# Optimization experiments

Hardware: AMD Instinct MI355X
Metric: run time of the kernel (lower is better)

Reference implementation:

```python
import jax, jax.numpy as jnp
import numpy as np

B, L, S, D, H, CTX = 2, 2048, 512, 1024, 16, 1024
HD = D // H
HID = 4 * D
EPS = 1e-6


def _ln(x):
    mu = jnp.mean(x, axis=-1, keepdims=True)
    var = jnp.mean((x - mu) ** 2, axis=-1, keepdims=True)
    return (x - mu) * jax.lax.rsqrt(var + EPS)


def _rotate_half(x):
    x1, x2 = jnp.split(x, 2, axis=-1)
    return jnp.concatenate([-x2, x1], axis=-1)


def _heads(t):  # [B,N,D] -> [B,H,N,HD]
    return t.reshape(t.shape[0], t.shape[1], H, HD).transpose(0, 2, 1, 3)


def _merge(t):  # [B,H,N,HD] -> [B,N,D]
    return t.transpose(0, 2, 1, 3).reshape(t.shape[0], t.shape[2], D)


def setup_inputs() -> dict:
    key = jax.random.key(0)
    ks = jax.random.split(key, 24)
    s = 0.02
    inp = {
        "x": jax.random.normal(ks[0], (B, L, D), jnp.float32),
        "timestep_emb": jax.random.normal(ks[1], (B, D), jnp.float32),
        "context_emb": jax.random.normal(ks[2], (B, S, CTX), jnp.float32),
        "rope_emb": jax.random.normal(ks[3], (L, HD), jnp.float32),
        # adaLN modulation: Linear(D -> 6D) with bias
        "w_mod": jax.random.normal(ks[4], (D, 6 * D), jnp.float32) * s,
        "b_mod": jnp.zeros((6 * D,), jnp.float32),
        # self-attention (no qkv bias, out has bias)
        "wq_s": jax.random.normal(ks[5], (D, D), jnp.float32) * s,
        "wk_s": jax.random.normal(ks[6], (D, D), jnp.float32) * s,
        "wv_s": jax.random.normal(ks[7], (D, D), jnp.float32) * s,
        "wo_s": jax.random.normal(ks[8], (D, D), jnp.float32) * s,
        "bo_s": jnp.zeros((D,), jnp.float32),
        # cross-attention (q/k/v no bias, out has bias)
        "wq_c": jax.random.normal(ks[9], (D, D), jnp.float32) * s,
        "wk_c": jax.random.normal(ks[10], (CTX, D), jnp.float32) * s,
        "wv_c": jax.random.normal(ks[11], (CTX, D), jnp.float32) * s,
        "wo_c": jax.random.normal(ks[12], (D, D), jnp.float32) * s,
        "bo_c": jnp.zeros((D,), jnp.float32),
        # MLP
        "w1": jax.random.normal(ks[13], (D, HID), jnp.float32) * s,
        "b1": jnp.zeros((HID,), jnp.float32),
        "w2": jax.random.normal(ks[14], (HID, D), jnp.float32) * s,
        "b2": jnp.zeros((D,), jnp.float32),
    }
    return inp


def reference(x, timestep_emb, context_emb, rope_emb,
              w_mod, b_mod,
              wq_s, wk_s, wv_s, wo_s, bo_s,
              wq_c, wk_c, wv_c, wo_c, bo_c,
              w1, b1, w2, b2):
    scale = HD ** -0.5
    # adaLN modulation from timestep embedding
    mods = jnp.split(timestep_emb @ w_mod + b_mod, 6, axis=-1)
    shift_msa, scale_msa, gate_msa, shift_mlp, scale_mlp, gate_mlp = mods

    # --- self-attention with RoPE ---
    nx = _ln(x) * (1.0 + scale_msa[:, None, :]) + shift_msa[:, None, :]
    q = _heads(nx @ wq_s)
    k = _heads(nx @ wk_s)
    v = _heads(nx @ wv_s)
    cos = jnp.cos(rope_emb)[None, None]  # [1,1,L,HD]
    sin = jnp.sin(rope_emb)[None, None]
    q = q * cos + _rotate_half(q) * sin
    k = k * cos + _rotate_half(k) * sin
    attn = jax.nn.softmax(jnp.einsum("bhqd,bhkd->bhqk", q, k) * scale, axis=-1)
    sa = _merge(jnp.einsum("bhqk,bhkd->bhqd", attn, v)) @ wo_s + bo_s
    x = x + gate_msa[:, None, :] * sa

    # --- cross-attention (no mask) ---
    nx = _ln(x)
    q = _heads(nx @ wq_c)
    k = _heads(context_emb @ wk_c)
    v = _heads(context_emb @ wv_c)
    attn = jax.nn.softmax(jnp.einsum("bhqd,bhkd->bhqk", q, k) * scale, axis=-1)
    ca = _merge(jnp.einsum("bhqk,bhkd->bhqd", attn, v)) @ wo_c + bo_c
    x = x + ca

    # --- MLP with modulation + gate ---
    nx = _ln(x) * (1.0 + scale_mlp[:, None, :]) + shift_mlp[:, None, :]
    h = jax.nn.gelu(nx @ w1 + b1, approximate=False)
    x = x + gate_mlp[:, None, :] * (h @ w2 + b2)
    return x
```

## Files before the change

kernel.cpp:

```cpp
#include <hip/hip_runtime.h>
#include <hip/hip_bf16.h>


typedef short short8 __attribute__((ext_vector_type(8)));
typedef float f32x4 __attribute__((ext_vector_type(4)));
typedef float f32x16 __attribute__((ext_vector_type(16)));

#define DEV __device__ __forceinline__

DEV unsigned short f2b(float f) {
  __hip_bfloat16 h = __float2bfloat16(f);
  return *reinterpret_cast<unsigned short*>(&h);
}
DEV float b2f(unsigned short u) {
  unsigned int x = ((unsigned int)u) << 16;
  return __builtin_bit_cast(float, x);
}
DEV unsigned int pk2(float lo, float hi) {
  unsigned int r;
  asm("v_cvt_pk_bf16_f32 %0, %1, %2" : "=v"(r) : "v"(lo), "v"(hi));
  return r;
}
DEV void vpsw(unsigned int& a, unsigned int& b) {
  asm("v_permlane32_swap_b32 %0, %1" : "+v"(a), "+v"(b));
}
DEV float max3f(float a, float b, float c) {
  float r;
  asm("v_max3_f32 %0, %1, %2, %3" : "=v"(r) : "v"(a), "v"(b), "v"(c));
  return r;
}

#define GLB(p) ((const __attribute__((address_space(1))) void*)(p))
#define LDSP(p) ((__attribute__((address_space(3))) void*)(p))

struct TCB { const float* in; unsigned short* out; float scale; };
struct PrepArgs {
  const float* wmod; const float* te; const float* bmod; float* mods;
  TCB sq[8];
  const float* w1; unsigned short* w1T;
  const float* w2; unsigned short* w2T;
  const float* ctx; unsigned short* ctxb;
  const float* rope; float2* cs;
};

__global__ __launch_bounds__(256) void prep(PrepArgs a) {
  __shared__ float t32[32][33];
  __shared__ float tes[2048];
  const int blk = blockIdx.x;
  const int tid = threadIdx.x;
  const int tx = tid & 31, ty = tid >> 5;
  if (blk < 24) {
    const int j = blk * 256 + tid;
    for (int u = tid; u < 2048; u += 256) tes[u] = a.te[u];
    __syncthreads();
    float a0 = 0.f, b0 = 0.f, a1 = 0.f, b1 = 0.f;
#pragma unroll 8
    for (int k = 0; k < 1024; k += 2) {
      float v0 = a.wmod[(size_t)k * 6144 + j];
      float v1 = a.wmod[(size_t)(k + 1) * 6144 + j];
      a0 += tes[k] * v0;
      b0 += tes[k + 1] * v1;
      a1 += tes[1024 + k] * v0;
      b1 += tes[1024 + k + 1] * v1;
    }
    float bm = a.bmod[j];
    a.mods[j] = a0 + b0 + bm;
    a.mods[6144 + j] = a1 + b1 + bm;
  } else if (blk < 16408) {
    const float* in;
    unsigned short* out;
    int R, C, gx, tile;
    float scale;
    if (blk < 8216) {
      int j = (blk - 24) >> 10;
      tile = (blk - 24) & 1023;
      in = a.sq[j].in; out = a.sq[j].out; scale = a.sq[j].scale;
      R = 1024; C = 1024; gx = 32;
    } else if (blk < 12312) {
      tile = blk - 8216;
      in = a.w1; out = a.w1T; R = 1024; C = 4096; gx = 128; scale = 1.f;
    } else {
      tile = blk - 12312;
      in = a.w2; out = a.w2T; R = 4096; C = 1024; gx = 32; scale = 1.f;
    }
    int bx = (tile % gx) * 32, by = (tile / gx) * 32;
#pragma unroll
    for (int i = ty; i < 32; i += 8)
      t32[i][tx] = in[(size_t)(by + i) * C + bx + tx];
    __syncthreads();
#pragma unroll
    for (int i = ty; i < 32; i += 8)
      out[(size_t)(bx + i) * R + by + tx] = f2b(t32[tx][i] * scale);
  } else if (blk < 18456) {
    int i = (blk - 16408) * 512 + tid * 2;
    float2 v = *(const float2*)&a.ctx[i];
    *(unsigned int*)&a.ctxb[i] = pk2(v.x, v.y);
  } else {
    int i = (blk - 18456) * 256 + tid;
    float v = a.rope[i];
    a.cs[i] = make_float2(cosf(v), sinf(v));
  }
}

template <int BF16IN>
__global__ __launch_bounds__(256) void ln_mod(
    const void* __restrict__ xin, const float* __restrict__ mods,
    unsigned short* __restrict__ out, int scale_ofs, int shift_ofs) {
  int row = blockIdx.x;
  int b = row >> 11;
  int tid = threadIdx.x;
  float vv[4];
  if constexpr (BF16IN) {
    const unsigned short* xr = (const unsigned short*)xin + (size_t)row * 1024;
    ushort4 u = ((const ushort4*)xr)[tid];
    vv[0] = b2f(u.x); vv[1] = b2f(u.y); vv[2] = b2f(u.z); vv[3] = b2f(u.w);
  } else {
    const float* xr = (const float*)xin + (size_t)row * 1024;
    float4 v = ((const float4*)xr)[tid];
    vv[0] = v.x; vv[1] = v.y; vv[2] = v.z; vv[3] = v.w;
  }
  float s = vv[0] + vv[1] + vv[2] + vv[3];
  float ss = vv[0] * vv[0] + vv[1] * vv[1] + vv[2] * vv[2] + vv[3] * vv[3];
#pragma unroll
  for (int off = 32; off >= 1; off >>= 1) {
    s += __shfl_down(s, off);
    ss += __shfl_down(ss, off);
  }
  __shared__ float red[8];
  int wave = tid >> 6, lane = tid & 63;
  if (lane == 0) { red[wave] = s; red[4 + wave] = ss; }
  __syncthreads();
  if (tid == 0) {
    float S = red[0] + red[1] + red[2] + red[3];
    float SS = red[4] + red[5] + red[6] + red[7];
    float mu = S * (1.f / 1024.f);
    red[0] = mu;
    red[1] = SS * (1.f / 1024.f) - mu * mu;
  }
  __syncthreads();
  float mu = red[0];
  float rs = rsqrtf(red[1] + 1e-6f);
  unsigned short o[4];
#pragma unroll
  for (int c = 0; c < 4; ++c) {
    int col = tid * 4 + c;
    float nv = (vv[c] - mu) * rs;
    if (scale_ofs >= 0)
      nv = nv * (1.f + mods[(size_t)b * 6144 + scale_ofs + col]) +
           mods[(size_t)b * 6144 + shift_ofs + col];
    o[c] = f2b(nv);
  }
  *(ushort4*)(&out[(size_t)row * 1024 + tid * 4]) = *(const ushort4*)o;
}

template <int EPI, int MI, int NJ>
DEV void gemm_epilogue(f32x4 (&acc)[MI][NJ], void* Cout, const float* bias,
                       const float* mods, int gate_ofs, const float* src,
                       int N, int rowsPerB, int m0, int n0, int wm, int wn,
                       int g, int r) {
#pragma unroll
  for (int i = 0; i < MI; ++i) {
#pragma unroll
    for (int j = 0; j < NJ; ++j) {
#pragma unroll
      for (int q = 0; q < 4; ++q) {
        size_t grow = (size_t)(m0 + wm + i * 16 + g * 4 + q);
        size_t gcol = (size_t)(n0 + wn + j * 16 + r);
        float v = acc[i][j][q];
        if constexpr (EPI == 0) {
          ((unsigned short*)Cout)[grow * N + gcol] = f2b(v);
        } else if constexpr (EPI == 1) {
          v += bias[gcol];
          float ge = 0.5f * v * (1.0f + erff(v * 0.70710678f));
          ((unsigned short*)Cout)[grow * N + gcol] = f2b(ge);
        } else if constexpr (EPI == 3) {
          size_t buf = gcol >> 10;
          ((unsigned short*)Cout)[buf * (4096ull * 1024) + grow * 1024 + (gcol & 1023)] = f2b(v);
        } else if constexpr (EPI == 5) {
          v += bias[gcol];
          float gate = 1.0f;
          if (gate_ofs >= 0)
            gate = mods[(grow / rowsPerB) * 6144 + gate_ofs + gcol];
          ((unsigned short*)Cout)[grow * N + gcol] =
              f2b(src[grow * N + gcol] + gate * v);
        } else if constexpr (EPI == 7) {
          v += bias[gcol];
          float gate = 1.0f;
          if (gate_ofs >= 0)
            gate = mods[(grow / rowsPerB) * 6144 + gate_ofs + gcol];
          float sv = b2f(((const unsigned short*)src)[grow * N + gcol]);
          ((float*)Cout)[grow * N + gcol] = sv + gate * v;
        } else {
          v += bias[gcol];
          float gate = 1.0f;
          if (gate_ofs >= 0)
            gate = mods[(grow / rowsPerB) * 6144 + gate_ofs + gcol];
          ((float*)Cout)[grow * N + gcol] = src[grow * N + gcol] + gate * v;
        }
      }
    }
  }
}

DEV void qkv_rope_epilogue(f32x4 (&acc)[4][4], unsigned short* Cout,
                           const float2* cs, int m0, int n0, int wm, int wn,
                           int g, int r) {
  const int buf = (n0 + wn) >> 10;
  const int colbase = (n0 + wn) & 1023;
  unsigned short* base = Cout + (size_t)buf * (4096ull * 1024);
#pragma unroll
  for (int i = 0; i < 4; ++i) {
#pragma unroll
    for (int q = 0; q < 4; ++q) {
      size_t grow = (size_t)(m0 + wm + i * 16 + g * 4 + q);
      unsigned short* orow = base + grow * 1024 + colbase + r;
      if (buf < 2) {
        int l = (int)(grow & 2047);
#pragma unroll
        for (int j = 0; j < 2; ++j) {
          int d = j * 16 + r;
          float2 a = cs[l * 64 + d];
          float2 bb = cs[l * 64 + d + 32];
          float x1 = acc[i][j][q], x2 = acc[i][j + 2][q];
          orow[j * 16] = f2b(x1 * a.x - x2 * a.y);
          orow[(j + 2) * 16] = f2b(x2 * bb.x + x1 * bb.y);
        }
      } else {
#pragma unroll
        for (int j = 0; j < 4; ++j) orow[j * 16] = f2b(acc[i][j][q]);
      }
    }
  }
}

template <int EPI>
__global__ __launch_bounds__(256, 2) void gemm_bt(
    const unsigned short* __restrict__ A, const unsigned short* __restrict__ Bt,
    void* __restrict__ Cout, const float* __restrict__ bias,
    const float* __restrict__ mods, int gate_ofs, const float* __restrict__ src,
    int M, int N, int K, int rowsPerB) {
  __shared__ unsigned short As[128 * 32];
  __shared__ unsigned short Bs[128 * 32];
  const int tid = threadIdx.x;
  const int wave = tid >> 6, lane = tid & 63;
  const int g = lane >> 4, r = lane & 15;
  const int m0 = blockIdx.y * 128, n0 = blockIdx.x * 128;
  const int wm = (wave >> 1) * 64, wn = (wave & 1) * 64;
  const int srow = lane >> 2;
  const int scol = (lane & 3) * 8;

  f32x4 acc[4][4] = {};

  for (int k0 = 0; k0 < K; k0 += 32) {
    __syncthreads();
#pragma unroll
    for (int cc = 0; cc < 4; ++cc) {
      int c = wave * 4 + cc;
      int isB = c >> 3;
      int cl = c & 7;
      int row = cl * 16 + srow;
      const unsigned short* gsrc =
          isB ? (Bt + (size_t)(n0 + row) * K + k0 + scol)
              : (A + (size_t)(m0 + row) * K + k0 + scol);
      unsigned short* ldst = (isB ? Bs : As) + cl * 512;
      __builtin_amdgcn_global_load_lds(GLB(gsrc), LDSP(ldst), 16, 0, 0);
    }
    __syncthreads();

    short8 bfr[4];
#pragma unroll
    for (int j = 0; j < 4; ++j)
      bfr[j] = *(const short8*)(&Bs[(wn + j * 16 + r) * 32 + g * 8]);
#pragma unroll
    for (int i = 0; i < 4; ++i) {
      short8 af = *(const short8*)(&As[(wm + i * 16 + r) * 32 + g * 8]);
#pragma unroll
      for (int j = 0; j < 4; ++j)
        acc[i][j] = __builtin_amdgcn_mfma_f32_16x16x32_bf16(af, bfr[j], acc[i][j], 0, 0, 0);
    }
  }
  gemm_epilogue<EPI, 4, 4>(acc, Cout, bias, mods, gate_ofs, src, N, rowsPerB,
                           m0, n0, wm, wn, g, r);
}

template <int EPI>
__global__ __launch_bounds__(256) void gemm_pipe(
    const unsigned short* __restrict__ A, const unsigned short* __restrict__ Bt,
    void* __restrict__ Cout, const float* __restrict__ bias,
    const float* __restrict__ mods, int gate_ofs, const float* __restrict__ src,
    int M, int N, int K, int rowsPerB, int mshift) {
  __shared__ unsigned short lds[4 * 16384];
  const int tid = threadIdx.x;
  const int wave = tid >> 6, lane = tid & 63;
  const int g = lane >> 4, r = lane & 15;
  const int flat = blockIdx.x;
  const int xcd = flat & 7, idx = flat >> 3;
  const int mt = xcd * (1 << mshift) + (idx & ((1 << mshift) - 1));
  const int nt = idx >> mshift;
  const int m0 = mt * 128, n0 = nt * 128;
  const int wm = (wave >> 1) * 64, wn = (wave & 1) * 64;
  const int srow8 = lane >> 3;
  const int sck = (lane & 7) ^ srow8;

  f32x4 acc[4][4] = {};

  auto stage = [&](int t, int bufi) {
    const int k0 = t * 64;
#pragma unroll
    for (int i = 0; i < 8; ++i) {
      int u = wave * 8 + i;
      int isB = u >> 4;
      int uu = u & 15;
      int rl = uu * 8 + srow8;
      const unsigned short* gsrc =
          (isB ? (Bt + (size_t)(n0 + rl) * K) : (A + (size_t)(m0 + rl) * K)) +
          k0 + sck * 8;
      unsigned short* dst = (unsigned short*)lds + bufi * 16384 + isB * 8192 + uu * 512;
      __builtin_amdgcn_global_load_lds(GLB(gsrc), LDSP(dst), 16, 0, 0);
    }
  };

  const int nt_k = K / 64;
  stage(0, 0);
  stage(1, 1);
  stage(2, 2);

  for (int t = 0; t < nt_k; ++t) {
    int rem = nt_k - t;
    if (rem >= 3) {
      asm volatile("s_waitcnt vmcnt(16)" ::: "memory");
    } else if (rem == 2) {
      asm volatile("s_waitcnt vmcnt(8)" ::: "memory");
    } else {
      asm volatile("s_waitcnt vmcnt(0)" ::: "memory");
    }
    __builtin_amdgcn_sched_barrier(0);
    __builtin_amdgcn_s_barrier();
    __builtin_amdgcn_sched_barrier(0);
    if (t + 3 < nt_k) stage(t + 3, (t + 3) & 3);

    const unsigned short* Ab = (const unsigned short*)lds + (t & 3) * 16384;
    const unsigned short* Bb = Ab + 8192;
#pragma unroll
    for (int ks = 0; ks < 2; ++ks) {
      short8 bfr[4];
#pragma unroll
      for (int j = 0; j < 4; ++j) {
        int row = wn + j * 16 + r;
        bfr[j] = *(const short8*)&Bb[row * 64 + ((g + ks * 4) ^ (r & 7)) * 8];
      }
#pragma unroll
      for (int i = 0; i < 4; ++i) {
        int row = wm + i * 16 + r;
        short8 af = *(const short8*)&Ab[row * 64 + ((g + ks * 4) ^ (r & 7)) * 8];
#pragma unroll
        for (int j = 0; j < 4; ++j)
          acc[i][j] = __builtin_amdgcn_mfma_f32_16x16x32_bf16(af, bfr[j], acc[i][j], 0, 0, 0);
      }
    }
  }
  if constexpr (EPI == 4) {
    qkv_rope_epilogue(acc, (unsigned short*)Cout, (const float2*)bias,
                      m0, n0, wm, wn, g, r);
  } else {
    gemm_epilogue<EPI, 4, 4>(acc, Cout, bias, mods, gate_ofs, src, N, rowsPerB,
                             m0, n0, wm, wn, g, r);
  }
}

template <int EPI>
__global__ __launch_bounds__(256) void gemm_p2(
    const unsigned short* __restrict__ A, const unsigned short* __restrict__ Bt,
    void* __restrict__ Cout, const float* __restrict__ bias,
    const float* __restrict__ mods, int gate_ofs, const float* __restrict__ src,
    int M, int N, int K, int rowsPerB, int ntn) {
  __shared__ unsigned short lds[3 * 12288];
  const int tid = threadIdx.x;
  const int wave = tid >> 6, lane = tid & 63;
  const int g = lane >> 4, r = lane & 15;
  const int flat = blockIdx.x;
  const int nt = flat % ntn, mt = flat / ntn;
  const int m0 = mt * 64, n0 = nt * 128;
  const int wm = (wave >> 1) * 32, wn = (wave & 1) * 64;
  const int srow8 = lane >> 3;
  const int sck = (lane & 7) ^ srow8;

  f32x4 acc[2][4] = {};

  auto stage = [&](int t, int bufi) {
    const int k0 = t * 64;
    unsigned short* base = (unsigned short*)lds + bufi * 12288;
#pragma unroll
    for (int i = 0; i < 2; ++i) {
      int u = wave * 2 + i;
      int rl = u * 8 + srow8;
      const unsigned short* gsrc = A + (size_t)(m0 + rl) * K + k0 + sck * 8;
      __builtin_amdgcn_global_load_lds(GLB(gsrc), LDSP(base + u * 512), 16, 0, 0);
    }
#pragma unroll
    for (int i = 0; i < 4; ++i) {
      int u = wave * 4 + i;
      int rl = u * 8 + srow8;
      const unsigned short* gsrc = Bt + (size_t)(n0 + rl) * K + k0 + sck * 8;
      __builtin_amdgcn_global_load_lds(GLB(gsrc), LDSP(base + 4096 + u * 512), 16, 0, 0);
    }
  };

  const int ntk = K / 64;
  stage(0, 0);
  stage(1, 1);
  int cbuf = 0, sbuf = 2;

  for (int t = 0; t < ntk; ++t) {
    if (t < ntk - 1) {
      asm volatile("s_waitcnt vmcnt(6)" ::: "memory");
    } else {
      asm volatile("s_waitcnt vmcnt(0)" ::: "memory");
    }
    __builtin_amdgcn_sched_barrier(0);
    __builtin_amdgcn_s_barrier();
    __builtin_amdgcn_sched_barrier(0);
    if (t + 2 < ntk) {
      stage(t + 2, sbuf);
      sbuf = (sbuf == 2) ? 0 : sbuf + 1;
    }

    const unsigned short* Ab = (const unsigned short*)lds + cbuf * 12288;
    const unsigned short* Bb = Ab + 4096;
#pragma unroll
    for (int ks = 0; ks < 2; ++ks) {
      short8 bfr[4];
#pragma unroll
      for (int j = 0; j < 4; ++j) {
        int row = wn + j * 16 + r;
        bfr[j] = *(const short8*)&Bb[row * 64 + ((g + ks * 4) ^ (r & 7)) * 8];
      }
#pragma unroll
      for (int i = 0; i < 2; ++i) {
        int row = wm + i * 16 + r;
        short8 af = *(const short8*)&Ab[row * 64 + ((g + ks * 4) ^ (r & 7)) * 8];
#pragma unroll
        for (int j = 0; j < 4; ++j)
          acc[i][j] = __builtin_amdgcn_mfma_f32_16x16x32_bf16(af, bfr[j], acc[i][j], 0, 0, 0);
      }
    }
    cbuf = (cbuf == 2) ? 0 : cbuf + 1;
  }
  gemm_epilogue<EPI, 2, 4>(acc, Cout, bias, mods, gate_ofs, src, N, rowsPerB,
                           m0, n0, wm, wn, g, r);
}

__global__ __launch_bounds__(256) void gemm_cross(
    const unsigned short* __restrict__ Anx, const unsigned short* __restrict__ Bq,
    unsigned short* __restrict__ Oq,
    const unsigned short* __restrict__ Actx, const unsigned short* __restrict__ Bkv,
    unsigned short* __restrict__ Okv) {
  __shared__ unsigned short lds[3 * 12288];
  const int tid = threadIdx.x;
  const int wave = tid >> 6, lane = tid & 63;
  const int g = lane >> 4, r = lane & 15;
  const bool iskv = blockIdx.x >= 512;
  const int flat = iskv ? (blockIdx.x - 512) : blockIdx.x;
  const int ntn = iskv ? 16 : 8;
  const unsigned short* A = iskv ? Actx : Anx;
  const unsigned short* Bt = iskv ? Bkv : Bq;
  const int nt = flat % ntn, mt = flat / ntn;
  const int m0 = mt * 64, n0 = nt * 128;
  const int K = 1024;
  const int wm = (wave >> 1) * 32, wn = (wave & 1) * 64;
  const int srow8 = lane >> 3;
  const int sck = (lane & 7) ^ srow8;

  f32x4 acc[2][4] = {};

  auto stage = [&](int t, int bufi) {
    const int k0 = t * 64;
    unsigned short* base = (unsigned short*)lds + bufi * 12288;
#pragma unroll
    for (int i = 0; i < 2; ++i) {
      int u = wave * 2 + i;
      int rl = u * 8 + srow8;
      const unsigned short* gsrc = A + (size_t)(m0 + rl) * K + k0 + sck * 8;
      __builtin_amdgcn_global_load_lds(GLB(gsrc), LDSP(base + u * 512), 16, 0, 0);
    }
#pragma unroll
    for (int i = 0; i < 4; ++i) {
      int u = wave * 4 + i;
      int rl = u * 8 + srow8;
      const unsigned short* gsrc = Bt + (size_t)(n0 + rl) * K + k0 + sck * 8;
      __builtin_amdgcn_global_load_lds(GLB(gsrc), LDSP(base + 4096 + u * 512), 16, 0, 0);
    }
  };

  const int ntk = K / 64;
  stage(0, 0);
  stage(1, 1);
  int cbuf = 0, sbuf = 2;

  for (int t = 0; t < ntk; ++t) {
    if (t < ntk - 1) {
      asm volatile("s_waitcnt vmcnt(6)" ::: "memory");
    } else {
      asm volatile("s_waitcnt vmcnt(0)" ::: "memory");
    }
    __builtin_amdgcn_sched_barrier(0);
    __builtin_amdgcn_s_barrier();
    __builtin_amdgcn_sched_barrier(0);
    if (t + 2 < ntk) {
      stage(t + 2, sbuf);
      sbuf = (sbuf == 2) ? 0 : sbuf + 1;
    }

    const unsigned short* Ab = (const unsigned short*)lds + cbuf * 12288;
    const unsigned short* Bb = Ab + 4096;
#pragma unroll
    for (int ks = 0; ks < 2; ++ks) {
      short8 bfr[4];
#pragma unroll
      for (int j = 0; j < 4; ++j) {
        int row = wn + j * 16 + r;
        bfr[j] = *(const short8*)&Bb[row * 64 + ((g + ks * 4) ^ (r & 7)) * 8];
      }
#pragma unroll
      for (int i = 0; i < 2; ++i) {
        int row = wm + i * 16 + r;
        short8 af = *(const short8*)&Ab[row * 64 + ((g + ks * 4) ^ (r & 7)) * 8];
#pragma unroll
        for (int j = 0; j < 4; ++j)
          acc[i][j] = __builtin_amdgcn_mfma_f32_16x16x32_bf16(af, bfr[j], acc[i][j], 0, 0, 0);
      }
    }
    cbuf = (cbuf == 2) ? 0 : cbuf + 1;
  }

#pragma unroll
  for (int i = 0; i < 2; ++i) {
#pragma unroll
    for (int j = 0; j < 4; ++j) {
#pragma unroll
      for (int q = 0; q < 4; ++q) {
        size_t grow = (size_t)(m0 + wm + i * 16 + g * 4 + q);
        size_t gcol = (size_t)(n0 + wn + j * 16 + r);
        float v = acc[i][j][q];
        if (iskv) {
          size_t buf = gcol >> 10;
          Okv[buf * (4096ull * 1024) + grow * 1024 + (gcol & 1023)] = f2b(v);
        } else {
          Oq[grow * 1024 + gcol] = f2b(v);
        }
      }
    }
  }
}

__global__ __launch_bounds__(256, 2) void flash2(
    const unsigned short* __restrict__ Q, const unsigned short* __restrict__ Kv,
    const unsigned short* __restrict__ Vv, unsigned short* __restrict__ O,
    int Lk) {
  __shared__ unsigned short lds[20480];
  const int tid = threadIdx.x, wave = tid >> 6, lane = tid & 63;
  const int hi = lane >> 5, lq = lane & 31;
  const int flat = blockIdx.x;
  const int xcd = flat & 7, rr = flat >> 3;
  const int gl = rr >> 4, qt = rr & 15;
  const int g = xcd * 4 + gl;
  const int h = g & 15, b = g >> 4;
  const int Lq = 2048, D = 1024;

  const unsigned short* Qbase =
      Q + ((size_t)b * Lq + qt * 128 + wave * 32 + lq) * D + h * 64;
  const unsigned short* Kbase = Kv + (size_t)b * Lk * D + h * 64;
  const unsigned short* Vbase = Vv + (size_t)b * Lk * D + h * 64;

  short8 qf[4];
#pragma unroll
  for (int kb = 0; kb < 4; ++kb)
    qf[kb] = *(const short8*)(Qbase + kb * 16 + hi * 8);

  const short8 ones = {0x3F80, 0x3F80, 0x3F80, 0x3F80, 0x3F80, 0x3F80, 0x3F80, 0x3F80};
  const f32x16 z16 = {};

  const int kr0 = tid >> 3, kc0 = tid & 7;
  const int kvp = tid >> 3, db = tid & 7;
  const int kch0 = (kc0 ^ (kr0 & 7) ^ (kr0 >> 3)) & 7;
  const int kch1 = kch0 ^ 4;
  const int f0 = (lq & 7) ^ (lq >> 3);
  const int swz0 = f0 << 4, swz1 = swz0 ^ 64;

  int vby[8];
#pragma unroll
  for (int e = 0; e < 8; ++e) {
    int d = db * 8 + e;
    vby[e] = d * 128 + ((kvp * 4) ^ (((e ^ db) & 7) << 4));
  }

  float m_run = -3.0e38f;
  f32x16 o0 = {}, o1 = {}, lacc = {};
  short8 vr0, vr1;
  short8 pbf[4];

  auto stageK = [&](int t, int bi) {
    const unsigned short* s0 = Kbase + (size_t)(t * 64 + kr0) * D + kch0 * 8;
    const unsigned short* s1 = Kbase + (size_t)(t * 64 + kr0 + 32) * D + kch1 * 8;
    __builtin_amdgcn_global_load_lds(GLB(s0), LDSP(&lds[bi * 4096 + wave * 512]), 16, 0, 0);
    __builtin_amdgcn_global_load_lds(GLB(s1), LDSP(&lds[bi * 4096 + 2048 + wave * 512]), 16, 0, 0);
  };
  auto loadV = [&](int t) {
    const unsigned short* v0 = Vbase + (size_t)(t * 64 + 2 * kvp) * D + db * 8;
    vr0 = *(const short8*)v0;
    vr1 = *(const short8*)(v0 + D);
  };
  auto writeV = [&](int t) {
    char* vt = (char*)&lds[12288 + (t & 1) * 4096];
    union { short8 s; unsigned int u[4]; } a, c;
    a.s = vr0; c.s = vr1;
#pragma unroll
    for (int k = 0; k < 4; ++k) {
      *(unsigned int*)(vt + vby[2 * k]) =
          __builtin_amdgcn_perm(c.u[k], a.u[k], 0x05040100u);
      *(unsigned int*)(vt + vby[2 * k + 1]) =
          __builtin_amdgcn_perm(c.u[k], a.u[k], 0x07060302u);
    }
  };
  auto qk = [&](int bi, f32x16& sa0, f32x16& sa1) {
    const unsigned short* K0 = &lds[bi * 4096];
    {
      int lo = hi * 16;
      short8 a0 = *(const short8*)&K0[lq * 64 + ((lo ^ swz0) >> 1)];
      short8 a1 = *(const short8*)&K0[(32 + lq) * 64 + ((lo ^ swz1) >> 1)];
      sa0 = __builtin_amdgcn_mfma_f32_32x32x16_bf16(a0, qf[0], z16, 0, 0, 0);
      sa1 = __builtin_amdgcn_mfma_f32_32x32x16_bf16(a1, qf[0], z16, 0, 0, 0);
    }
#pragma unroll
    for (int ks = 1; ks < 4; ++ks) {
      int lo = ks * 32 + hi * 16;
      short8 a0 = *(const short8*)&K0[lq * 64 + ((lo ^ swz0) >> 1)];
      short8 a1 = *(const short8*)&K0[(32 + lq) * 64 + ((lo ^ swz1) >> 1)];
      sa0 = __builtin_amdgcn_mfma_f32_32x32x16_bf16(a0, qf[ks], sa0, 0, 0, 0);
      sa1 = __builtin_amdgcn_mfma_f32_32x32x16_bf16(a1, qf[ks], sa1, 0, 0, 0);
    }
  };
  auto finish = [&](f32x16& s0a, f32x16& s1a) {
    float tm[8];
#pragma unroll
    for (int i = 0; i < 8; ++i)
      tm[i] = fmaxf(max3f(s0a[i], s0a[i + 8], s1a[i]), s1a[i + 8]);
    float x = max3f(tm[0], tm[1], tm[2]);
    float y = max3f(tm[3], tm[4], tm[5]);
    float pm = fmaxf(max3f(tm[6], tm[7], x), y);
    {
      unsigned int ua = __builtin_bit_cast(unsigned int, pm), ub = ua;
      vpsw(ua, ub);
      pm = fmaxf(__builtin_bit_cast(float, ua), __builtin_bit_cast(float, ub));
    }
    if (__any(pm - m_run > 8.0f)) {
      float mnew = fmaxf(m_run, pm);
      float alpha = exp2f(m_run - mnew);
      lacc[0] *= alpha;
#pragma unroll
      for (int i = 0; i < 16; ++i) { o0[i] *= alpha; o1[i] *= alpha; }
      m_run = mnew;
    }
    float mc = m_run;
#pragma unroll
    for (int i = 0; i < 16; ++i) s0a[i] = exp2f(s0a[i] - mc);
#pragma unroll
    for (int i = 0; i < 16; ++i) s1a[i] = exp2f(s1a[i] - mc);
#pragma unroll
    for (int kb = 0; kb < 4; ++kb) {
      int bb = (kb & 1) * 8;
      float p0, p1, p2, p3, p4, p5, p6, p7;
      if (kb < 2) {
        p0 = s0a[bb + 0]; p1 = s0a[bb + 1]; p2 = s0a[bb + 2]; p3 = s0a[bb + 3];
        p4 = s0a[bb + 4]; p5 = s0a[bb + 5]; p6 = s0a[bb + 6]; p7 = s0a[bb + 7];
      } else {
        p0 = s1a[bb + 0]; p1 = s1a[bb + 1]; p2 = s1a[bb + 2]; p3 = s1a[bb + 3];
        p4 = s1a[bb + 4]; p5 = s1a[bb + 5]; p6 = s1a[bb + 6]; p7 = s1a[bb + 7];
      }
      unsigned int u0 = pk2(p0, p1), u1 = pk2(p2, p3);
      unsigned int u2 = pk2(p4, p5), u3 = pk2(p6, p7);
      vpsw(u0, u2);
      vpsw(u1, u3);
      union { unsigned int u[4]; short8 s; } fr;
      fr.u[0] = u0; fr.u[1] = u1; fr.u[2] = u2; fr.u[3] = u3;
      pbf[kb] = fr.s;
    }
  };
  auto pv = [&](int t) {
    const unsigned short* V0 = &lds[12288 + (t & 1) * 4096];
    __builtin_amdgcn_s_setprio(1);
#pragma unroll
    for (int kb = 0; kb < 4; ++kb) {
      int lo = kb * 32 + hi * 16;
      short8 vf0 = *(const short8*)&V0[lq * 64 + ((lo ^ swz0) >> 1)];
      short8 vf1 = *(const short8*)&V0[(32 + lq) * 64 + ((lo ^ swz1) >> 1)];
      o0 = __builtin_amdgcn_mfma_f32_32x32x16_bf16(vf0, pbf[kb], o0, 0, 0, 0);
      o1 = __builtin_amdgcn_mfma_f32_32x32x16_bf16(vf1, pbf[kb], o1, 0, 0, 0);
      lacc = __builtin_amdgcn_mfma_f32_32x32x16_bf16(ones, pbf[kb], lacc, 0, 0, 0);
    }
    __builtin_amdgcn_s_setprio(0);
  };

  const int nkt = Lk / 64;

  stageK(0, 0);
  loadV(0);
  writeV(0);
  stageK(1, 1);
  __syncthreads();

  f32x16 sA0, sA1, sB0, sB1;
  qk(0, sA0, sA1);

  auto pstep = [&](int t, f32x16& n0, f32x16& n1, f32x16& p0, f32x16& p1) {
    const int tq = t + 1;
    if (tq < nkt) {
      loadV(tq);
      if (tq + 1 < nkt) stageK(tq + 1, (tq + 1) % 3);
      qk(tq % 3, n0, n1);
    }
    finish(p0, p1);
    if (tq < nkt) writeV(tq);
    pv(t);
    __syncthreads();
  };

  for (int t = 0; t < nkt; t += 2) {
    pstep(t, sB0, sB1, sA0, sA1);
    pstep(t + 1, sA0, sA1, sB0, sB1);
  }

  float rl = 1.0f / lacc[0];
  unsigned short* os = &lds[wave * 2048];
#pragma unroll
  for (int t = 0; t < 2; ++t) {
#pragma unroll
    for (int c = 0; c < 4; ++c) {
      int dbase = 32 * t + 8 * c + 4 * hi;
      float v0 = (t ? o1[4 * c + 0] : o0[4 * c + 0]) * rl;
      float v1 = (t ? o1[4 * c + 1] : o0[4 * c + 1]) * rl;
      float v2 = (t ? o1[4 * c + 2] : o0[4 * c + 2]) * rl;
      float v3 = (t ? o1[4 * c + 3] : o0[4 * c + 3]) * rl;
      int by0 = lq * 128 + ((dbase * 2) ^ ((lq & 7) << 4));
      int by1 = lq * 128 + (((dbase + 2) * 2) ^ ((lq & 7) << 4));
      *(unsigned int*)((char*)os + by0) = pk2(v0, v1);
      *(unsigned int*)((char*)os + by1) = pk2(v2, v3);
    }
  }
  int q2 = lane >> 1;
  unsigned short* orow =
      O + ((size_t)b * Lq + qt * 128 + wave * 32 + q2) * D + h * 64;
#pragma unroll
  for (int j = 0; j < 4; ++j) {
    int j2 = (lane & 1) * 4 + j;
    int byr = q2 * 128 + ((j2 * 16) ^ ((q2 & 7) << 4));
    short8 vv = *(const short8*)((char*)os + byr);
    *(short8*)(orow + j2 * 8) = vv;
  }
}

extern "C" void kernel_launch(void* const* d_in, const int* in_sizes, int n_in,
                              void* d_out, int out_size, void* d_ws, size_t ws_size,
                              hipStream_t stream) {
  (void)in_sizes; (void)n_in; (void)out_size; (void)ws_size;
  const float* x_in = (const float*)d_in[0];
  const float* te   = (const float*)d_in[1];
  const float* ctx  = (const float*)d_in[2];
  const float* rope = (const float*)d_in[3];
  const float* wmod = (const float*)d_in[4];
  const float* bmod = (const float*)d_in[5];
  const float* wqs  = (const float*)d_in[6];
  const float* wks  = (const float*)d_in[7];
  const float* wvs  = (const float*)d_in[8];
  const float* wos  = (const float*)d_in[9];
  const float* bos  = (const float*)d_in[10];
  const float* wqc  = (const float*)d_in[11];
  const float* wkc  = (const float*)d_in[12];
  const float* wvc  = (const float*)d_in[13];
  const float* woc  = (const float*)d_in[14];
  const float* boc  = (const float*)d_in[15];
  const float* w1   = (const float*)d_in[16];
  const float* b1   = (const float*)d_in[17];
  const float* w2   = (const float*)d_in[18];
  const float* b2   = (const float*)d_in[19];
  float* out = (float*)d_out;

  char* w = (char*)d_ws;
  size_t o = 0;
  auto alloc = [&](size_t bytes) {
    char* p = w + o;
    o = (o + bytes + 255) & ~(size_t)255;
    return p;
  };
  unsigned short* wqsT  = (unsigned short*)alloc(1024ull * 1024 * 2);
  unsigned short* wksT  = (unsigned short*)alloc(1024ull * 1024 * 2);
  unsigned short* wvsT  = (unsigned short*)alloc(1024ull * 1024 * 2);
  unsigned short* wosT  = (unsigned short*)alloc(1024ull * 1024 * 2);
  unsigned short* wqcT  = (unsigned short*)alloc(1024ull * 1024 * 2);
  unsigned short* wkcT  = (unsigned short*)alloc(1024ull * 1024 * 2);
  unsigned short* wvcT  = (unsigned short*)alloc(1024ull * 1024 * 2);
  unsigned short* wocT  = (unsigned short*)alloc(1024ull * 1024 * 2);
  unsigned short* w1T   = (unsigned short*)alloc(4096ull * 1024 * 2);
  unsigned short* w2T   = (unsigned short*)alloc(1024ull * 4096 * 2);
  float* modsb = (float*)alloc(2ull * 6144 * 4);
  float2* csT  = (float2*)alloc(2048ull * 64 * 8);
  unsigned short* nx   = (unsigned short*)alloc(4096ull * 1024 * 2);
  unsigned short* ctxb = (unsigned short*)alloc(1024ull * 1024 * 2);
  unsigned short* qb = (unsigned short*)alloc(4096ull * 1024 * 2);
  unsigned short* kb = (unsigned short*)alloc(4096ull * 1024 * 2);
  unsigned short* vb = (unsigned short*)alloc(4096ull * 1024 * 2);
  unsigned short* ao = (unsigned short*)alloc(4096ull * 1024 * 2);
  unsigned short* xwb = (unsigned short*)alloc(4096ull * 1024 * 2);
  float* xw = (float*)alloc(4096ull * 1024 * 4);
  unsigned short* hbuf = qb;

  const float c1 = 0.125f * 1.4426950408889634f;

  PrepArgs pa;
  pa.wmod = wmod; pa.te = te; pa.bmod = bmod; pa.mods = modsb;
  pa.sq[0] = {wqs, wqsT, c1};
  pa.sq[1] = {wks, wksT, 1.0f};
  pa.sq[2] = {wvs, wvsT, 1.0f};
  pa.sq[3] = {wos, wosT, 1.0f};
  pa.sq[4] = {wqc, wqcT, 1.0f};
  pa.sq[5] = {wkc, wkcT, c1};
  pa.sq[6] = {wvc, wvcT, 1.0f};
  pa.sq[7] = {woc, wocT, 1.0f};
  pa.w1 = w1; pa.w1T = w1T;
  pa.w2 = w2; pa.w2T = w2T;
  pa.ctx = ctx; pa.ctxb = ctxb;
  pa.rope = rope; pa.cs = csT;
  prep<<<18968, 256, 0, stream>>>(pa);

  ln_mod<0><<<4096, 256, 0, stream>>>(x_in, modsb, nx, 1024, 0);
  gemm_pipe<4><<<768, 256, 0, stream>>>(nx, wqsT, qb, (const float*)csT, nullptr, -1, nullptr, 4096, 3072, 1024, 2048, 2);
  flash2<<<512, 256, 0, stream>>>(qb, kb, vb, ao, 2048);
  gemm_p2<5><<<512, 256, 0, stream>>>(ao, wosT, xwb, bos, modsb, 2048, x_in, 4096, 1024, 1024, 2048, 8);

  ln_mod<1><<<4096, 256, 0, stream>>>(xwb, modsb, nx, -1, -1);
  gemm_cross<<<768, 256, 0, stream>>>(nx, wqcT, qb, ctxb, wkcT, kb);
  flash2<<<512, 256, 0, stream>>>(qb, kb, vb, ao, 512);
  gemm_p2<7><<<512, 256, 0, stream>>>(ao, wocT, xw, boc, modsb, -1, (const float*)xwb, 4096, 1024, 1024, 2048, 8);

  ln_mod<0><<<4096, 256, 0, stream>>>(xw, modsb, nx, 4096, 3072);
  gemm_bt<1><<<dim3(32, 32), 256, 0, stream>>>(nx, w1T, hbuf, b1, nullptr, -1, nullptr, 4096, 4096, 1024, 2048);
  gemm_p2<2><<<512, 256, 0, stream>>>(hbuf, w2T, out, b2, modsb, 5120, xw, 4096, 1024, 4096, 2048, 8);
}
```

Measured before the change: 387.2 us.

## Compute cross-attention K/V projection inside self-attention flash kernel as extra blocks

The context K/V projection depends only on the context embedding, so it now runs as 128 extra blocks appended to the self-attention flash kernel launch. Those blocks do a simple 128x128-tiled GEMM and write into new dedicated kc/vc buffers. The Q-only cross projection then uses the existing gemm_p2 kernel, and the separate gemm_cross launch is dropped. This overlaps the small K/V GEMM with attention and shortens the work between LN and cross-attention, at the cost of a less pipelined, single-buffered GEMM path and LDS/register pressure inside flash2.

```diff
diff --git a/kernel.cpp b/kernel.cpp
--- a/kernel.cpp
+++ b/kernel.cpp
@@ -450,115 +450,70 @@
                            m0, n0, wm, wn, g, r);
 }
 
-__global__ __launch_bounds__(256) void gemm_cross(
-    const unsigned short* __restrict__ Anx, const unsigned short* __restrict__ Bq,
-    unsigned short* __restrict__ Oq,
-    const unsigned short* __restrict__ Actx, const unsigned short* __restrict__ Bkv,
-    unsigned short* __restrict__ Okv) {
-  __shared__ unsigned short lds[3 * 12288];
-  const int tid = threadIdx.x;
-  const int wave = tid >> 6, lane = tid & 63;
-  const int g = lane >> 4, r = lane & 15;
-  const bool iskv = blockIdx.x >= 512;
-  const int flat = iskv ? (blockIdx.x - 512) : blockIdx.x;
-  const int ntn = iskv ? 16 : 8;
-  const unsigned short* A = iskv ? Actx : Anx;
-  const unsigned short* Bt = iskv ? Bkv : Bq;
-  const int nt = flat % ntn, mt = flat / ntn;
-  const int m0 = mt * 64, n0 = nt * 128;
-  const int K = 1024;
-  const int wm = (wave >> 1) * 32, wn = (wave & 1) * 64;
-  const int srow8 = lane >> 3;
-  const int sck = (lane & 7) ^ srow8;
-
-  f32x4 acc[2][4] = {};
-
-  auto stage = [&](int t, int bufi) {
-    const int k0 = t * 64;
-    unsigned short* base = (unsigned short*)lds + bufi * 12288;
-#pragma unroll
-    for (int i = 0; i < 2; ++i) {
-      int u = wave * 2 + i;
-      int rl = u * 8 + srow8;
-      const unsigned short* gsrc = A + (size_t)(m0 + rl) * K + k0 + sck * 8;
-      __builtin_amdgcn_global_load_lds(GLB(gsrc), LDSP(base + u * 512), 16, 0, 0);
-    }
-#pragma unroll
-    for (int i = 0; i < 4; ++i) {
-      int u = wave * 4 + i;
-      int rl = u * 8 + srow8;
-      const unsigned short* gsrc = Bt + (size_t)(n0 + rl) * K + k0 + sck * 8;
-      __builtin_amdgcn_global_load_lds(GLB(gsrc), LDSP(base + 4096 + u * 512), 16, 0, 0);
-    }
-  };
-
-  const int ntk = K / 64;
-  stage(0, 0);
-  stage(1, 1);
-  int cbuf = 0, sbuf = 2;
-
-  for (int t = 0; t < ntk; ++t) {
-    if (t < ntk - 1) {
-      asm volatile("s_waitcnt vmcnt(6)" ::: "memory");
-    } else {
-      asm volatile("s_waitcnt vmcnt(0)" ::: "memory");
-    }
-    __builtin_amdgcn_sched_barrier(0);
-    __builtin_amdgcn_s_barrier();
-    __builtin_amdgcn_sched_barrier(0);
-    if (t + 2 < ntk) {
-      stage(t + 2, sbuf);
-      sbuf = (sbuf == 2) ? 0 : sbuf + 1;
-    }
-
-    const unsigned short* Ab = (const unsigned short*)lds + cbuf * 12288;
-    const unsigned short* Bb = Ab + 4096;
-#pragma unroll
-    for (int ks = 0; ks < 2; ++ks) {
-      short8 bfr[4];
-#pragma unroll
-      for (int j = 0; j < 4; ++j) {
-        int row = wn + j * 16 + r;
-        bfr[j] = *(const short8*)&Bb[row * 64 + ((g + ks * 4) ^ (r & 7)) * 8];
-      }
-#pragma unroll
-      for (int i = 0; i < 2; ++i) {
-        int row = wm + i * 16 + r;
-        short8 af = *(const short8*)&Ab[row * 64 + ((g + ks * 4) ^ (r & 7)) * 8];
-#pragma unroll
-        for (int j = 0; j < 4; ++j)
-          acc[i][j] = __builtin_amdgcn_mfma_f32_16x16x32_bf16(af, bfr[j], acc[i][j], 0, 0, 0);
-      }
-    }
-    cbuf = (cbuf == 2) ? 0 : cbuf + 1;
-  }
-
-#pragma unroll
-  for (int i = 0; i < 2; ++i) {
-#pragma unroll
-    for (int j = 0; j < 4; ++j) {
-#pragma unroll
-      for (int q = 0; q < 4; ++q) {
-        size_t grow = (size_t)(m0 + wm + i * 16 + g * 4 + q);
-        size_t gcol = (size_t)(n0 + wn + j * 16 + r);
-        float v = acc[i][j][q];
-        if (iskv) {
-          size_t buf = gcol >> 10;
-          Okv[buf * (4096ull * 1024) + grow * 1024 + (gcol & 1023)] = f2b(v);
-        } else {
-          Oq[grow * 1024 + gcol] = f2b(v);
-        }
-      }
-    }
-  }
-}
-
 __global__ __launch_bounds__(256, 2) void flash2(
     const unsigned short* __restrict__ Q, const unsigned short* __restrict__ Kv,
     const unsigned short* __restrict__ Vv, unsigned short* __restrict__ O,
-    int Lk) {
+    int Lk,
+    const unsigned short* __restrict__ Actx,
+    const unsigned short* __restrict__ Bkv,
+    unsigned short* __restrict__ Okv) {
   __shared__ unsigned short lds[20480];
   const int tid = threadIdx.x, wave = tid >> 6, lane = tid & 63;
+
+  if (blockIdx.x >= 512) {
+    const int gblk = blockIdx.x - 512;
+    const int m0 = (gblk >> 4) * 128, n0 = (gblk & 15) * 128;
+    const int g = lane >> 4, r = lane & 15;
+    const int wm = (wave >> 1) * 64, wn = (wave & 1) * 64;
+    const int srow = lane >> 2;
+    const int scol = (lane & 3) * 8;
+    unsigned short* As = lds;
+    unsigned short* Bs = lds + 4096;
+    f32x4 acc[4][4] = {};
+    for (int k0 = 0; k0 < 1024; k0 += 32) {
+      __syncthreads();
+#pragma unroll
+      for (int cc = 0; cc < 4; ++cc) {
+        int c = wave * 4 + cc;
+        int isB = c >> 3;
+        int cl = c & 7;
+        int row = cl * 16 + srow;
+        const unsigned short* gsrc =
+            isB ? (Bkv + (size_t)(n0 + row) * 1024 + k0 + scol)
+                : (Actx + (size_t)(m0 + row) * 1024 + k0 + scol);
+        unsigned short* ldst = (isB ? Bs : As) + cl * 512;
+        __builtin_amdgcn_global_load_lds(GLB(gsrc), LDSP(ldst), 16, 0, 0);
+      }
+      __syncthreads();
+      short8 bfr[4];
+#pragma unroll
+      for (int j = 0; j < 4; ++j)
+        bfr[j] = *(const short8*)(&Bs[(wn + j * 16 + r) * 32 + g * 8]);
+#pragma unroll
+      for (int i = 0; i < 4; ++i) {
+        short8 af = *(const short8*)(&As[(wm + i * 16 + r) * 32 + g * 8]);
+#pragma unroll
+        for (int j = 0; j < 4; ++j)
+          acc[i][j] = __builtin_amdgcn_mfma_f32_16x16x32_bf16(af, bfr[j], acc[i][j], 0, 0, 0);
+      }
+    }
+#pragma unroll
+    for (int i = 0; i < 4; ++i) {
+#pragma unroll
+      for (int j = 0; j < 4; ++j) {
+#pragma unroll
+        for (int q = 0; q < 4; ++q) {
+          size_t grow = (size_t)(m0 + wm + i * 16 + g * 4 + q);
+          size_t gcol = (size_t)(n0 + wn + j * 16 + r);
+          size_t buf = gcol >> 10;
+          Okv[buf * (1024ull * 1024) + grow * 1024 + (gcol & 1023)] =
+              f2b(acc[i][j][q]);
+        }
+      }
+    }
+    return;
+  }
+
   const int hi = lane >> 5, lq = lane & 31;
   const int flat = blockIdx.x;
   const int xcd = flat & 7, rr = flat >> 3;
@@ -810,6 +765,8 @@
   unsigned short* kb = (unsigned short*)alloc(4096ull * 1024 * 2);
   unsigned short* vb = (unsigned short*)alloc(4096ull * 1024 * 2);
   unsigned short* ao = (unsigned short*)alloc(4096ull * 1024 * 2);
+  unsigned short* kcb = (unsigned short*)alloc(1024ull * 1024 * 2);
+  unsigned short* vcb = (unsigned short*)alloc(1024ull * 1024 * 2);
   unsigned short* xwb = (unsigned short*)alloc(4096ull * 1024 * 2);
   float* xw = (float*)alloc(4096ull * 1024 * 4);
   unsigned short* hbuf = qb;
@@ -834,12 +791,12 @@
 
   ln_mod<0><<<4096, 256, 0, stream>>>(x_in, modsb, nx, 1024, 0);
   gemm_pipe<4><<<768, 256, 0, stream>>>(nx, wqsT, qb, (const float*)csT, nullptr, -1, nullptr, 4096, 3072, 1024, 2048, 2);
-  flash2<<<512, 256, 0, stream>>>(qb, kb, vb, ao, 2048);
+  flash2<<<640, 256, 0, stream>>>(qb, kb, vb, ao, 2048, ctxb, wkcT, kcb);
   gemm_p2<5><<<512, 256, 0, stream>>>(ao, wosT, xwb, bos, modsb, 2048, x_in, 4096, 1024, 1024, 2048, 8);
 
   ln_mod<1><<<4096, 256, 0, stream>>>(xwb, modsb, nx, -1, -1);
-  gemm_cross<<<768, 256, 0, stream>>>(nx, wqcT, qb, ctxb, wkcT, kb);
-  flash2<<<512, 256, 0, stream>>>(qb, kb, vb, ao, 512);
+  gemm_p2<0><<<512, 256, 0, stream>>>(nx, wqcT, qb, nullptr, nullptr, -1, nullptr, 4096, 1024, 1024, 2048, 8);
+  flash2<<<512, 256, 0, stream>>>(qb, kcb, vcb, ao, 512, nullptr, nullptr, nullptr);
   gemm_p2<7><<<512, 256, 0, stream>>>(ao, wocT, xw, boc, modsb, -1, (const float*)xwb, 4096, 1024, 1024, 2048, 8);
 
   ln_mod<0><<<4096, 256, 0, stream>>>(xw, modsb, nx, 4096, 3072);
```

Result: no change. 387.6 us (+0.1%).
